# Optimization experiments

Hardware: AMD Instinct MI355X
Metric: run time of the kernel (lower is better)

The kernel has to match this reference:

```python
import jax, jax.numpy as jnp
import numpy as np

D_IN, D_HIDDEN, DT_RANK = 768, 16, 48


def setup_inputs() -> dict:
    key = jax.random.key(0)
    ks = jax.random.split(key, 6)
    b, l, d, n, r = 2, 2048, D_IN, D_HIDDEN, DT_RANK
    p = 3 * n + 2 * d + 2 * r  # x_proj output width = 1680
    x = jax.random.normal(ks[0], (b, l, d), jnp.float32)
    z = jax.random.normal(ks[1], (b, d, l), jnp.float32)
    # A_log = log(repeat(arange(1, n+1), 'n -> d n'))
    A_log = jnp.log(jnp.broadcast_to(jnp.arange(1, n + 1, dtype=jnp.float32), (d, n)))
    D = jnp.ones((d,), jnp.float32)
    W_xproj = jax.random.normal(ks[2], (p, d), jnp.float32) / np.sqrt(d)
    W_dt = jax.random.normal(ks[3], (d, r), jnp.float32) / np.sqrt(r)
    # dt bias init: inverse-softplus of dt ~ LogUniform(1e-3, 1e-1)
    dt = jnp.exp(jax.random.uniform(ks[4], (d,)) * (np.log(0.1) - np.log(0.001)) + np.log(0.001))
    dt = jnp.clip(dt, 1e-4)
    b_dt = dt + jnp.log(-jnp.expm1(-dt))
    return dict(x=x, z=z, A_log=A_log, D=D, W_xproj=W_xproj, W_dt=W_dt, b_dt=b_dt)


def reference(x, z, A_log, D, W_xproj, W_dt, b_dt):
    b, l, d = x.shape
    n = A_log.shape[1]
    r = W_dt.shape[1]
    A = -jnp.exp(A_log)                      # (d, n)
    proj = x @ W_xproj.T                     # (b, l, 3n + 2d + 2r)
    Bm = proj[..., :n]                       # (b, l, n)  input matrix B
    Cm = proj[..., 2 * n:3 * n]              # (b, l, n)  output matrix C
    dt = proj[..., 3 * n + 2 * d:3 * n + 2 * d + r]   # (b, l, r)
    # NOTE: source adds dt_proj bias via the Linear AND again via delta_bias -> 2*b_dt
    delta = jax.nn.softplus(dt @ W_dt.T + 2.0 * b_dt)  # (b, l, d)
    dA = jnp.exp(delta[..., None] * A)                  # (b, l, d, n)
    dBu = (delta * x)[..., None] * Bm[:, :, None, :]    # (b, l, d, n)

    def step(h, inp):
        dA_t, dBu_t, C_t = inp
        h = dA_t * h + dBu_t                 # (b, d, n)
        return h, jnp.einsum('bdn,bn->bd', h, C_t)

    h0 = jnp.zeros((b, d, n), x.dtype)
    _, ys = jax.lax.scan(step, h0, (jnp.swapaxes(dA, 0, 1), jnp.swapaxes(dBu, 0, 1), jnp.swapaxes(Cm, 0, 1)))
    y = jnp.swapaxes(ys, 0, 1) + x * D       # (b, l, d)  + skip D*u
    zl = jnp.swapaxes(z, 1, 2)               # z is (b, d, l) -> (b, l, d)
    return y * (zl * jax.nn.sigmoid(zl))     # gate with silu(z)
```

## Files before the change

kernel.cpp:

```cpp
#include <hip/hip_runtime.h>
#include <math.h>

#define BATCH 2
#define LSEQ  2048
#define DIM   768
#define NST   16
#define RDT   48
#define BL    (BATCH*LSEQ)
#define NCHUNK 32
#define CLEN   (LSEQ/NCHUNK)
#define CPAD   68
#define NPACK  (CLEN/4)
#define LP4    (LSEQ/4)

typedef __attribute__((ext_vector_type(8))) short short8;
typedef __attribute__((ext_vector_type(4))) float float4e;

__device__ __forceinline__ ushort f2bf(float f) {
    union { float f; unsigned u; } v; v.f = f;
    unsigned u = v.u;
    u += 0x7fffu + ((u >> 16) & 1u);
    return (ushort)(u >> 16);
}

__global__ __launch_bounds__(256) void pack_kernel(
        const float* __restrict__ x, const float* __restrict__ Wx,
        ushort* __restrict__ xbf, float* __restrict__ xT,
        ushort* __restrict__ Wbf) {
    if (blockIdx.y == 12) {
        const int blk = blockIdx.z * 32 + blockIdx.x;
        for (int idx = blk * 256 + threadIdx.x; idx < 80 * DIM; idx += 64 * 256) {
            const int j = idx / DIM;
            const int k = idx - j * DIM;
            const int row = (j < 16) ? j : ((j < 32) ? (j + 16) : (j + 1552));
            Wbf[idx] = f2bf(Wx[(size_t)row * DIM + k]);
        }
        return;
    }
    __shared__ float tile[64][65];
    const int r0 = blockIdx.x * 64;
    const int c0 = blockIdx.y * 64;
    const int b  = blockIdx.z;
    const int tx = threadIdx.x & 63;
    const int ty = threadIdx.x >> 6;
    #pragma unroll
    for (int k = 0; k < 16; ++k) {
        const int r = ty * 16 + k;
        const size_t gidx = ((size_t)b * LSEQ + (r0 + r)) * DIM + c0 + tx;
        const float v = x[gidx];
        tile[r][tx] = v;
        xbf[gidx] = f2bf(v);
    }
    __syncthreads();
    #pragma unroll
    for (int k = 0; k < 16; ++k) {
        const int r = ty * 16 + k;
        xT[((size_t)b * DIM + (c0 + r)) * LSEQ + r0 + tx] = tile[tx][r];
    }
}

__global__ __launch_bounds__(64) void proj_gemm_kernel(
        const ushort* __restrict__ xbf, const ushort* __restrict__ Wbf,
        float* __restrict__ Bpk, float* __restrict__ Cpk,
        float* __restrict__ dtpT) {
    const int m0   = blockIdx.x * 16;
    const int lane = threadIdx.x;
    const int col  = lane & 15;
    const int quad = lane >> 4;

    const short* A  = (const short*)xbf + (size_t)(m0 + col) * DIM + quad * 8;
    const short* Bw = (const short*)Wbf;

    float4e acc[5] = {};
    #pragma unroll 6
    for (int kk = 0; kk < 24; ++kk) {
        const short8 a = *(const short8*)(A + kk * 32);
        #pragma unroll
        for (int nt = 0; nt < 5; ++nt) {
            const short8 bf = *(const short8*)(Bw + (size_t)(nt * 16 + col) * DIM + kk * 32 + quad * 8);
            acc[nt] = __builtin_amdgcn_mfma_f32_16x16x32_bf16(a, bf, acc[nt], 0, 0, 0);
        }
    }

    const int b  = m0 >> 11;
    const int t0 = m0 & 2047;
    const size_t pk4 = ((size_t)(b * LP4 + (t0 >> 2) + quad)) * NST + col;
    ((float4*)Bpk)[pk4] = *(float4*)&acc[0];
    ((float4*)Cpk)[pk4] = *(float4*)&acc[1];
    #pragma unroll
    for (int nt = 2; nt < 5; ++nt) {
        const int r = (nt - 2) * 16 + col;
        *(float4*)(dtpT + ((size_t)(b * RDT + r)) * LSEQ + t0 + quad * 4) = *(float4*)&acc[nt];
    }
}

__global__ __launch_bounds__(256) void xpose_kernel(
        const float* __restrict__ in, float* __restrict__ out, int R, int C) {
    __shared__ float tile[64][65];
    const int r0 = blockIdx.x * 64;
    const int c0 = blockIdx.y * 64;
    const int b  = blockIdx.z;
    const int tx = threadIdx.x & 63;
    const int ty = threadIdx.x >> 6;
    #pragma unroll
    for (int k = 0; k < 16; ++k) {
        const int r = ty * 16 + k;
        tile[r][tx] = in[((size_t)b * R + (r0 + r)) * C + c0 + tx];
    }
    __syncthreads();
    #pragma unroll
    for (int k = 0; k < 16; ++k) {
        const int r = ty * 16 + k;
        out[((size_t)b * C + (c0 + r)) * R + r0 + tx] = tile[tx][r];
    }
}

__global__ __launch_bounds__(512) void scan_kernel(
        const float* __restrict__ xT, const float* __restrict__ z,
        const float* __restrict__ A_log, const float* __restrict__ Dp,
        const float* __restrict__ Bpk, const float* __restrict__ Cpk,
        const float* __restrict__ dtpT, const float* __restrict__ Wdt,
        const float* __restrict__ bdt, float* __restrict__ yT) {
    __shared__ float sdel[NCHUNK * CPAD];
    __shared__ float sx[NCHUNK * CPAD];
    __shared__ float sP[NCHUNK][NST];
    __shared__ float sq[NCHUNK][NST];
    __shared__ float sw[RDT];

    const int tid = threadIdx.x;
    const int ch = blockIdx.x;
    const int b = ch / DIM;
    const int d = ch % DIM;
    const size_t row = (size_t)ch * LSEQ;

    if (tid < RDT) sw[tid] = Wdt[(size_t)d * RDT + tid];
    {
        const float4 xv4 = ((const float4*)(xT + row))[tid];
        ((float4*)sx)[(tid >> 4) * (CPAD / 4) + (tid & 15)] = xv4;
    }
    __syncthreads();

    {
        const float bb = 2.0f * bdt[d];
        const float* dbase = dtpT + (size_t)b * RDT * LSEQ;
        float4 acc = make_float4(bb, bb, bb, bb);
        #pragma unroll 3
        for (int k4 = 0; k4 < RDT / 4; ++k4) {
            const float4 wv = ((const float4*)sw)[k4];
            #pragma unroll
            for (int j = 0; j < 4; ++j) {
                const int k = k4 * 4 + j;
                const float wk = (j == 0) ? wv.x : (j == 1) ? wv.y : (j == 2) ? wv.z : wv.w;
                const float4 v = ((const float4*)(dbase + (size_t)k * LSEQ))[tid];
                acc.x = fmaf(v.x, wk, acc.x);
                acc.y = fmaf(v.y, wk, acc.y);
                acc.z = fmaf(v.z, wk, acc.z);
                acc.w = fmaf(v.w, wk, acc.w);
            }
        }
        float4 sp;
        sp.x = (acc.x > 20.f) ? acc.x : __logf(1.f + __expf(acc.x));
        sp.y = (acc.y > 20.f) ? acc.y : __logf(1.f + __expf(acc.y));
        sp.z = (acc.z > 20.f) ? acc.z : __logf(1.f + __expf(acc.z));
        sp.w = (acc.w > 20.f) ? acc.w : __logf(1.f + __expf(acc.w));
        ((float4*)sdel)[(tid >> 4) * (CPAD / 4) + (tid & 15)] = sp;
    }
    __syncthreads();

    const int g = tid >> 4;
    const int n = tid & 15;
    const float Aln = -__expf(A_log[d * NST + n]);
    const float4* Bg = (const float4*)Bpk + ((size_t)(b * LP4 + g * NPACK) * NST + n);
    const float4* Cg = (const float4*)Cpk + ((size_t)(b * LP4 + g * NPACK) * NST + n);
    const float* dchunk = sdel + g * CPAD;
    const float* xchunk = sx + g * CPAD;

    {
        float h = 0.f, Ptot = 1.f;
        float4 Bn_ = Bg[0];
        #pragma unroll 4
        for (int p = 0; p < NPACK; ++p) {
            const float4 B4 = Bn_;
            if (p < NPACK - 1) Bn_ = Bg[(p + 1) * NST];
            const float4 dl = *(const float4*)(dchunk + 4 * p);
            const float4 xv = *(const float4*)(xchunk + 4 * p);
            const float u0 = dl.x * xv.x * B4.x, u1 = dl.y * xv.y * B4.y;
            const float u2 = dl.z * xv.z * B4.z, u3 = dl.w * xv.w * B4.w;
            const float e0  = __expf(Aln * dl.x), dA1 = __expf(Aln * dl.y);
            const float dA2 = __expf(Aln * dl.z), dA3 = __expf(Aln * dl.w);
            float s = u0;
            s = fmaf(dA1, s, u1); s = fmaf(dA2, s, u2); s = fmaf(dA3, s, u3);
            const float E3 = ((e0 * dA1) * (dA2 * dA3));
            h = fmaf(E3, h, s);
            Ptot *= E3;
        }
        sP[g][n] = Ptot;
        sq[g][n] = h;
    }
    __syncthreads();

    {
        float Pc = sP[g][n], qc = sq[g][n];
        #pragma unroll
        for (int s = 1; s < NCHUNK; s <<= 1) {
            float Pp = 1.f, qp = 0.f;
            if (g >= s) { Pp = sP[g - s][n]; qp = sq[g - s][n]; }
            __syncthreads();
            qc = fmaf(Pc, qp, qc);
            Pc *= Pp;
            sP[g][n] = Pc; sq[g][n] = qc;
            __syncthreads();
        }
    }

    {
        float h = (g == 0) ? 0.f : sq[g - 1][n];
        const float Dd = Dp[d];
        float* ybuf = sdel;
        float4 Bn_ = Bg[0];
        float4 Cn_ = Cg[0];
        #pragma unroll 4
        for (int p = 0; p < NPACK; ++p) {
            const float4 B4 = Bn_, C4 = Cn_;
            if (p < NPACK - 1) { Bn_ = Bg[(p + 1) * NST]; Cn_ = Cg[(p + 1) * NST]; }
            const float4 dl = *(const float4*)(dchunk + 4 * p);
            const float4 xv = *(const float4*)(xchunk + 4 * p);
            const float u0 = dl.x * xv.x * B4.x, u1 = dl.y * xv.y * B4.y;
            const float u2 = dl.z * xv.z * B4.z, u3 = dl.w * xv.w * B4.w;
            const float E0  = __expf(Aln * dl.x), dA1 = __expf(Aln * dl.y);
            const float dA2 = __expf(Aln * dl.z), dA3 = __expf(Aln * dl.w);
            const float E1 = E0 * dA1, E2 = E1 * dA2, E3 = E2 * dA3;
            const float s0 = u0;
            const float s1 = fmaf(dA1, s0, u1);
            const float s2 = fmaf(dA2, s1, u2);
            const float s3 = fmaf(dA3, s2, u3);
            const float h0 = fmaf(E0, h, s0);
            const float h1 = fmaf(E1, h, s1);
            const float h2 = fmaf(E2, h, s2);
            const float h3 = fmaf(E3, h, s3);
            h = h3;
            float p0 = h0 * C4.x, p1 = h1 * C4.y, p2 = h2 * C4.z, p3 = h3 * C4.w;
            p0 += __shfl_xor(p0, 1); p0 += __shfl_xor(p0, 2);
            p1 += __shfl_xor(p1, 1); p1 += __shfl_xor(p1, 2);
            p2 += __shfl_xor(p2, 1); p2 += __shfl_xor(p2, 2);
            p3 += __shfl_xor(p3, 1); p3 += __shfl_xor(p3, 2);
            float v = (n & 1) ? ((n & 2) ? p3 : p1) : ((n & 2) ? p2 : p0);
            v += __shfl_xor(v, 4);
            v += __shfl_xor(v, 8);
            if (n < 4) {
                const float xvn = (n == 0) ? xv.x : (n == 1) ? xv.y : (n == 2) ? xv.z : xv.w;
                ybuf[g * CPAD + 4 * p + n] = fmaf(xvn, Dd, v);
            }
        }
    }
    __syncthreads();

    {
        const float* zrow = z + row;
        float* yrow = yT + row;
        #pragma unroll
        for (int i = tid; i < LSEQ; i += 512) {
            const float zv = zrow[i];
            const float sig = 1.0f / (1.0f + __expf(-zv));
            yrow[i] = sdel[(i >> 6) * CPAD + (i & 63)] * zv * sig;
        }
    }
}

extern "C" void kernel_launch(void* const* d_in, const int* in_sizes, int n_in,
                              void* d_out, int out_size, void* d_ws, size_t ws_size,
                              hipStream_t stream) {
    const float* x     = (const float*)d_in[0];
    const float* z     = (const float*)d_in[1];
    const float* A_log = (const float*)d_in[2];
    const float* D     = (const float*)d_in[3];
    const float* Wx    = (const float*)d_in[4];
    const float* Wdt   = (const float*)d_in[5];
    const float* bdt   = (const float*)d_in[6];
    float* out = (float*)d_out;

    float* ws    = (float*)d_ws;
    float* Bpk   = ws;
    float* Cpk   = Bpk + (size_t)BATCH * LP4 * NST * 4;
    float* dtpT  = Cpk + (size_t)BATCH * LP4 * NST * 4;
    float* xT    = dtpT + (size_t)BATCH * RDT * LSEQ;
    float* yT    = xT;
    ushort* xbf  = (ushort*)(xT + (size_t)BATCH * DIM * LSEQ);
    ushort* Wbf  = xbf + (size_t)BATCH * LSEQ * DIM;

    hipLaunchKernelGGL(pack_kernel, dim3(LSEQ / 64, DIM / 64 + 1, BATCH), dim3(256), 0, stream,
                       x, Wx, xbf, xT, Wbf);
    hipLaunchKernelGGL(proj_gemm_kernel, dim3(BL / 16), dim3(64), 0, stream,
                       xbf, Wbf, Bpk, Cpk, dtpT);
    hipLaunchKernelGGL(scan_kernel, dim3(BATCH * DIM), dim3(512), 0, stream,
                       xT, z, A_log, D, Bpk, Cpk, dtpT, Wdt, bdt, yT);
    hipLaunchKernelGGL(xpose_kernel, dim3(DIM / 64, LSEQ / 64, BATCH), dim3(256), 0, stream,
                       yT, out, DIM, LSEQ);
}
```

Measured before the change: 154.6 us.

## Vectorize transpose kernels and precompute delta*x, use exp2 in scan

The pack and transpose kernels move to float4 loads and stores with a 68-float padded shared tile, and bf16 output is written as packed pairs. The scan kernel precomputes delta*x once into a new shared buffer, replaces __expf with a native exp2 on a log2e-prescaled A, and moves the D skip term into the final gating loop. Together these aim to cut memory transactions in the transpose kernels and arithmetic in the serial scan loops, at the cost of extra shared memory in the scan kernel. The padded float4 tile layout may also introduce shared-memory bank conflicts on the strided column reads.

```diff
diff --git a/kernel.cpp b/kernel.cpp
--- a/kernel.cpp
+++ b/kernel.cpp
@@ -12,6 +12,7 @@
 #define CPAD   68
 #define NPACK  (CLEN/4)
 #define LP4    (LSEQ/4)
+#define L2E    1.4426950408889634f
 
 typedef __attribute__((ext_vector_type(8))) short short8;
 typedef __attribute__((ext_vector_type(4))) float float4e;
@@ -21,6 +22,9 @@
     unsigned u = v.u;
     u += 0x7fffu + ((u >> 16) & 1u);
     return (ushort)(u >> 16);
+}
+__device__ __forceinline__ unsigned pk2bf(float a, float b) {
+    return (unsigned)f2bf(a) | ((unsigned)f2bf(b) << 16);
 }
 
 __global__ __launch_bounds__(256) void pack_kernel(
@@ -37,25 +41,33 @@
         }
         return;
     }
-    __shared__ float tile[64][65];
+    __shared__ float tile[64 * 68];
     const int r0 = blockIdx.x * 64;
     const int c0 = blockIdx.y * 64;
     const int b  = blockIdx.z;
-    const int tx = threadIdx.x & 63;
-    const int ty = threadIdx.x >> 6;
-    #pragma unroll
-    for (int k = 0; k < 16; ++k) {
-        const int r = ty * 16 + k;
-        const size_t gidx = ((size_t)b * LSEQ + (r0 + r)) * DIM + c0 + tx;
-        const float v = x[gidx];
-        tile[r][tx] = v;
-        xbf[gidx] = f2bf(v);
-    }
-    __syncthreads();
-    #pragma unroll
-    for (int k = 0; k < 16; ++k) {
-        const int r = ty * 16 + k;
-        xT[((size_t)b * DIM + (c0 + r)) * LSEQ + r0 + tx] = tile[tx][r];
+    const int tid = threadIdx.x;
+    const int c4 = tid & 15;
+    const int rb = tid >> 4;
+    #pragma unroll
+    for (int rr = 0; rr < 4; ++rr) {
+        const int row = rr * 16 + rb;
+        const size_t gbase = ((size_t)b * LSEQ + (r0 + row)) * DIM + c0;
+        const float4 v = *(const float4*)(x + gbase + c4 * 4);
+        *(float4*)&tile[row * 68 + c4 * 4] = v;
+        const uint2 bf = make_uint2(pk2bf(v.x, v.y), pk2bf(v.z, v.w));
+        *(uint2*)(xbf + gbase + c4 * 4) = bf;
+    }
+    __syncthreads();
+    const int c  = tid & 63;
+    const int l0 = (tid >> 6) * 16;
+    float* dst = xT + ((size_t)b * DIM + c0 + c) * LSEQ + r0 + l0;
+    #pragma unroll
+    for (int q = 0; q < 4; ++q) {
+        const float4 v = make_float4(tile[(l0 + 4*q + 0) * 68 + c],
+                                     tile[(l0 + 4*q + 1) * 68 + c],
+                                     tile[(l0 + 4*q + 2) * 68 + c],
+                                     tile[(l0 + 4*q + 3) * 68 + c]);
+        *(float4*)(dst + 4 * q) = v;
     }
 }
 
@@ -96,22 +108,30 @@
 
 __global__ __launch_bounds__(256) void xpose_kernel(
         const float* __restrict__ in, float* __restrict__ out, int R, int C) {
-    __shared__ float tile[64][65];
+    __shared__ float tile[64 * 68];
     const int r0 = blockIdx.x * 64;
     const int c0 = blockIdx.y * 64;
     const int b  = blockIdx.z;
-    const int tx = threadIdx.x & 63;
-    const int ty = threadIdx.x >> 6;
-    #pragma unroll
-    for (int k = 0; k < 16; ++k) {
-        const int r = ty * 16 + k;
-        tile[r][tx] = in[((size_t)b * R + (r0 + r)) * C + c0 + tx];
-    }
-    __syncthreads();
-    #pragma unroll
-    for (int k = 0; k < 16; ++k) {
-        const int r = ty * 16 + k;
-        out[((size_t)b * C + (c0 + r)) * R + r0 + tx] = tile[tx][r];
+    const int tid = threadIdx.x;
+    const int c4 = tid & 15;
+    const int rb = tid >> 4;
+    #pragma unroll
+    for (int rr = 0; rr < 4; ++rr) {
+        const int row = rr * 16 + rb;
+        const float4 v = *(const float4*)(in + ((size_t)b * R + (r0 + row)) * C + c0 + c4 * 4);
+        *(float4*)&tile[row * 68 + c4 * 4] = v;
+    }
+    __syncthreads();
+    const int c  = tid & 63;
+    const int l0 = (tid >> 6) * 16;
+    float* dst = out + ((size_t)b * C + (c0 + c)) * R + r0 + l0;
+    #pragma unroll
+    for (int q = 0; q < 4; ++q) {
+        const float4 v = make_float4(tile[(l0 + 4*q + 0) * 68 + c],
+                                     tile[(l0 + 4*q + 1) * 68 + c],
+                                     tile[(l0 + 4*q + 2) * 68 + c],
+                                     tile[(l0 + 4*q + 3) * 68 + c]);
+        *(float4*)(dst + 4 * q) = v;
     }
 }
 
@@ -122,6 +142,7 @@
         const float* __restrict__ dtpT, const float* __restrict__ Wdt,
         const float* __restrict__ bdt, float* __restrict__ yT) {
     __shared__ float sdel[NCHUNK * CPAD];
+    __shared__ float sdlx[NCHUNK * CPAD];
     __shared__ float sx[NCHUNK * CPAD];
     __shared__ float sP[NCHUNK][NST];
     __shared__ float sq[NCHUNK][NST];
@@ -134,10 +155,8 @@
     const size_t row = (size_t)ch * LSEQ;
 
     if (tid < RDT) sw[tid] = Wdt[(size_t)d * RDT + tid];
-    {
-        const float4 xv4 = ((const float4*)(xT + row))[tid];
-        ((float4*)sx)[(tid >> 4) * (CPAD / 4) + (tid & 15)] = xv4;
-    }
+    const float4 xv4 = ((const float4*)(xT + row))[tid];
+    ((float4*)sx)[(tid >> 4) * (CPAD / 4) + (tid & 15)] = xv4;
     __syncthreads();
 
     {
@@ -163,17 +182,20 @@
         sp.y = (acc.y > 20.f) ? acc.y : __logf(1.f + __expf(acc.y));
         sp.z = (acc.z > 20.f) ? acc.z : __logf(1.f + __expf(acc.z));
         sp.w = (acc.w > 20.f) ? acc.w : __logf(1.f + __expf(acc.w));
-        ((float4*)sdel)[(tid >> 4) * (CPAD / 4) + (tid & 15)] = sp;
+        const int sidx = (tid >> 4) * (CPAD / 4) + (tid & 15);
+        ((float4*)sdel)[sidx] = sp;
+        ((float4*)sdlx)[sidx] = make_float4(sp.x * xv4.x, sp.y * xv4.y,
+                                            sp.z * xv4.z, sp.w * xv4.w);
     }
     __syncthreads();
 
     const int g = tid >> 4;
     const int n = tid & 15;
-    const float Aln = -__expf(A_log[d * NST + n]);
+    const float Aln2 = -__expf(A_log[d * NST + n]) * L2E;
     const float4* Bg = (const float4*)Bpk + ((size_t)(b * LP4 + g * NPACK) * NST + n);
     const float4* Cg = (const float4*)Cpk + ((size_t)(b * LP4 + g * NPACK) * NST + n);
-    const float* dchunk = sdel + g * CPAD;
-    const float* xchunk = sx + g * CPAD;
+    const float* dchunk  = sdel + g * CPAD;
+    const float* uxchunk = sdlx + g * CPAD;
 
     {
         float h = 0.f, Ptot = 1.f;
@@ -183,11 +205,13 @@
             const float4 B4 = Bn_;
             if (p < NPACK - 1) Bn_ = Bg[(p + 1) * NST];
             const float4 dl = *(const float4*)(dchunk + 4 * p);
-            const float4 xv = *(const float4*)(xchunk + 4 * p);
-            const float u0 = dl.x * xv.x * B4.x, u1 = dl.y * xv.y * B4.y;
-            const float u2 = dl.z * xv.z * B4.z, u3 = dl.w * xv.w * B4.w;
-            const float e0  = __expf(Aln * dl.x), dA1 = __expf(Aln * dl.y);
-            const float dA2 = __expf(Aln * dl.z), dA3 = __expf(Aln * dl.w);
+            const float4 ux = *(const float4*)(uxchunk + 4 * p);
+            const float u0 = ux.x * B4.x, u1 = ux.y * B4.y;
+            const float u2 = ux.z * B4.z, u3 = ux.w * B4.w;
+            const float e0  = __builtin_amdgcn_exp2f(Aln2 * dl.x);
+            const float dA1 = __builtin_amdgcn_exp2f(Aln2 * dl.y);
+            const float dA2 = __builtin_amdgcn_exp2f(Aln2 * dl.z);
+            const float dA3 = __builtin_amdgcn_exp2f(Aln2 * dl.w);
             float s = u0;
             s = fmaf(dA1, s, u1); s = fmaf(dA2, s, u2); s = fmaf(dA3, s, u3);
             const float E3 = ((e0 * dA1) * (dA2 * dA3));
@@ -215,7 +239,6 @@
 
     {
         float h = (g == 0) ? 0.f : sq[g - 1][n];
-        const float Dd = Dp[d];
         float* ybuf = sdel;
         float4 Bn_ = Bg[0];
         float4 Cn_ = Cg[0];
@@ -224,11 +247,13 @@
             const float4 B4 = Bn_, C4 = Cn_;
             if (p < NPACK - 1) { Bn_ = Bg[(p + 1) * NST]; Cn_ = Cg[(p + 1) * NST]; }
             const float4 dl = *(const float4*)(dchunk + 4 * p);
-            const float4 xv = *(const float4*)(xchunk + 4 * p);
-            const float u0 = dl.x * xv.x * B4.x, u1 = dl.y * xv.y * B4.y;
-            const float u2 = dl.z * xv.z * B4.z, u3 = dl.w * xv.w * B4.w;
-            const float E0  = __expf(Aln * dl.x), dA1 = __expf(Aln * dl.y);
-            const float dA2 = __expf(Aln * dl.z), dA3 = __expf(Aln * dl.w);
+            const float4 ux = *(const float4*)(uxchunk + 4 * p);
+            const float u0 = ux.x * B4.x, u1 = ux.y * B4.y;
+            const float u2 = ux.z * B4.z, u3 = ux.w * B4.w;
+            const float E0  = __builtin_amdgcn_exp2f(Aln2 * dl.x);
+            const float dA1 = __builtin_amdgcn_exp2f(Aln2 * dl.y);
+            const float dA2 = __builtin_amdgcn_exp2f(Aln2 * dl.z);
+            const float dA3 = __builtin_amdgcn_exp2f(Aln2 * dl.w);
             const float E1 = E0 * dA1, E2 = E1 * dA2, E3 = E2 * dA3;
             const float s0 = u0;
             const float s1 = fmaf(dA1, s0, u1);
@@ -247,22 +272,21 @@
             float v = (n & 1) ? ((n & 2) ? p3 : p1) : ((n & 2) ? p2 : p0);
             v += __shfl_xor(v, 4);
             v += __shfl_xor(v, 8);
-            if (n < 4) {
-                const float xvn = (n == 0) ? xv.x : (n == 1) ? xv.y : (n == 2) ? xv.z : xv.w;
-                ybuf[g * CPAD + 4 * p + n] = fmaf(xvn, Dd, v);
-            }
-        }
-    }
-    __syncthreads();
-
-    {
+            if (n < 4) ybuf[g * CPAD + 4 * p + n] = v;
+        }
+    }
+    __syncthreads();
+
+    {
+        const float Dd = Dp[d];
         const float* zrow = z + row;
         float* yrow = yT + row;
         #pragma unroll
         for (int i = tid; i < LSEQ; i += 512) {
+            const int idx = (i >> 6) * CPAD + (i & 63);
             const float zv = zrow[i];
             const float sig = 1.0f / (1.0f + __expf(-zv));
-            yrow[i] = sdel[(i >> 6) * CPAD + (i & 63)] * zv * sig;
+            yrow[i] = fmaf(sx[idx], Dd, sdel[idx]) * zv * sig;
         }
     }
 }
```

Result: no change. 156.2 us (+1.0%).
